# Kernel optimization log

Measured on AMD Instinct MI355X. Metric: run time of the kernel, lower is better.

The kernel has to match this reference:

```python
import jax, jax.numpy as jnp
import numpy as np

T, B, I, H, LBL = 200, 1024, 128, 128, 4


def setup_inputs() -> dict:
    key = jax.random.key(0)
    ks = jax.random.split(key, 14)
    si = 1.0 / np.sqrt(I)
    sh = 1.0 / np.sqrt(H)
    inputs = jax.random.normal(ks[0], (T, B, I), jnp.float32)
    lengths = jnp.maximum(jax.random.randint(ks[1], (B,), 1, T + 1), LBL).astype(jnp.int32)
    return {
        "inputs": inputs,
        "lengths": lengths,
        "Wih_g": jax.random.normal(ks[2], (3 * H, I), jnp.float32) * si,
        "Whh_g": jax.random.normal(ks[3], (3 * H, H), jnp.float32) * sh,
        "bih_g": jax.random.normal(ks[4], (3 * H,), jnp.float32) * sh,
        "bhh_g": jax.random.normal(ks[5], (3 * H,), jnp.float32) * sh,
        "Wih_l": jax.random.normal(ks[6], (3 * H, I), jnp.float32) * si,
        "Whh_l": jax.random.normal(ks[7], (3 * H, H), jnp.float32) * sh,
        "bih_l": jax.random.normal(ks[8], (3 * H,), jnp.float32) * sh,
        "bhh_l": jax.random.normal(ks[9], (3 * H,), jnp.float32) * sh,
        "A1": jax.random.normal(ks[10], (H, H), jnp.float32) * sh,
        "A2": jax.random.normal(ks[11], (H, H), jnp.float32) * sh,
        "v1": jax.random.normal(ks[12], (1, H), jnp.float32) * sh,
        "label_len": LBL,
    }


def gru(x, Wih, Whh, bih, bhh):
    # x: [T, B, I] time-major. PyTorch GRU cell semantics.
    Bq, Hq = x.shape[1], Whh.shape[1]
    gi_all = jnp.einsum('tbi,gi->tbg', x, Wih) + bih  # precompute input projections [T,B,3H]
    def step(h, gi):
        gh = h @ Whh.T + bhh
        ir, iz, inn = jnp.split(gi, 3, axis=-1)
        hr, hz, hn = jnp.split(gh, 3, axis=-1)
        r = jax.nn.sigmoid(ir + hr)
        z = jax.nn.sigmoid(iz + hz)
        n = jnp.tanh(inn + r * hn)
        h = (1.0 - z) * n + z * h
        return h, h
    h0 = jnp.zeros((Bq, Hq), x.dtype)
    _, hs = jax.lax.scan(step, h0, gi_all)
    return hs  # [T, B, H]


def reference(inputs, lengths, Wih_g, Whh_g, bih_g, bhh_g,
              Wih_l, Whh_l, bih_l, bhh_l, A1, A2, v1, label_len):
    h_g = gru(inputs, Wih_g, Whh_g, bih_g, bhh_g)  # [T,B,H]
    h_l = gru(inputs, Wih_l, Whh_l, bih_l, bhh_l)  # [T,B,H]
    # attention score per step s: v1(sigmoid(A1 h_l + A2 h_g)), query-independent
    pre = jax.nn.sigmoid(jnp.einsum('tbh,gh->tbg', h_l, A1) +
                         jnp.einsum('tbh,gh->tbg', h_g, A2))
    scores = jnp.einsum('tbg,og->tbo', pre, v1)  # [T,B,1]
    # per-t output = cumsum_{s<=t}(score*h_l) + h_g[t]
    out = jnp.cumsum(scores * h_l, axis=0) + h_g  # [T,B,H]
    out_b = jnp.transpose(out, (1, 0, 2))  # [B,T,H]
    # gather last label_len timesteps of each sequence: h[b,k] = out[L_b-label_len+k, b]
    idx = lengths[:, None].astype(jnp.int32) - label_len + jnp.arange(label_len, dtype=jnp.int32)[None, :]
    idx = jnp.clip(idx, 0, out_b.shape[1] - 1)  # [B, label_len]
    h = jnp.take_along_axis(out_b, idx[:, :, None], axis=1)  # [B, label_len, H]
    return h
```

## Files before the change

### kernel.cpp

```cpp
#include <hip/hip_runtime.h>
#include <stdint.h>


typedef __attribute__((ext_vector_type(8))) short short8;
typedef __attribute__((ext_vector_type(4))) float float4v;

#define LDS_BARRIER() asm volatile("s_waitcnt lgkmcnt(0)\n\ts_barrier" ::: "memory")

__device__ inline float bf2f(unsigned short u){
  union { unsigned int i; float f; } v; v.i = ((unsigned int)u) << 16; return v.f;
}
__device__ inline unsigned short f2bf(float f){
  union { float f; unsigned int i; } v; v.f = f;
  unsigned int x = v.i;
  return (unsigned short)((x + 0x7fffu + ((x >> 16) & 1u)) >> 16);
}
__device__ inline unsigned int cvt_pk_bf16(float a, float b){
  unsigned int r;
  asm("v_cvt_pk_bf16_f32 %0, %1, %2" : "=v"(r) : "v"(a), "v"(b));
  return r;
}
__device__ inline float sigm(float x){ return __builtin_amdgcn_rcpf(1.0f + __expf(-x)); }

__global__ void k_prep(unsigned short* zs, float* cum,
                       const float* A1, const float* A2, unsigned short* a12)
{
  int i = blockIdx.x * blockDim.x + threadIdx.x;
  zs[i] = 0;
  cum[i] = 0.0f;
  if (i < 32768) {
    a12[i] = f2bf((i < 16384) ? A1[i] : A2[i - 16384]);
  }
}

union __align__(16) LdsU {
  struct { unsigned short hbuf[2][16][136]; unsigned short xbuf[2][16][136]; } scan;
  struct { unsigned short M1[128][136]; unsigned short M2[128][136]; } sc;
  struct { unsigned short hlL[50 * 512]; float scL[4][50]; } cm;
};

__global__ __launch_bounds__(512, 2) void k_fat(
    const float* __restrict__ x,
    const float* __restrict__ Wih_g, const float* __restrict__ Whh_g,
    const float* __restrict__ bih_g, const float* __restrict__ bhh_g,
    const float* __restrict__ Wih_l, const float* __restrict__ Whh_l,
    const float* __restrict__ bih_l, const float* __restrict__ bhh_l,
    const unsigned short* __restrict__ a12, const float* __restrict__ v1,
    const int* __restrict__ lengths,
    unsigned short* __restrict__ hl, unsigned short* __restrict__ hg,
    const unsigned short* __restrict__ zs,
    float* __restrict__ score, float* __restrict__ cum, float* __restrict__ out,
    int scan_t0, int score_t0, int cum_t0)
{
  __shared__ LdsU lds;
  int tid = threadIdx.x;
  int bid = blockIdx.x;

  if (bid < 128) {
    if (scan_t0 < 0) return;
    const int tc = 50;
    int t0 = scan_t0;
    auto& hbuf = lds.scan.hbuf;
    auto& xbuf = lds.scan.xbuf;

    int w = tid >> 6, L = tid & 63, l15 = L & 15, q = L >> 4;
    int gru = bid & 1;
    int b0 = (bid >> 1) * 16;
    const float* Wih = gru ? Wih_l : Wih_g;
    const float* Whh = gru ? Whh_l : Whh_g;
    const float* bih = gru ? bih_l : bih_g;
    const float* bhh = gru ? bhh_l : bhh_g;
    unsigned short* myseq = gru ? hl : hg;

    int col = w * 16 + l15;

    short8 Wi[3][4], Wh[3][4];
    #pragma unroll
    for (int G = 0; G < 3; G++) {
      int row = G * 128 + col;
      #pragma unroll
      for (int kf = 0; kf < 4; kf++) {
        const float4* p0 = (const float4*)(Wih + (size_t)row * 128 + kf * 32 + q * 8);
        const float4* p1 = (const float4*)(Whh + (size_t)row * 128 + kf * 32 + q * 8);
        float4 a0 = p0[0], a1 = p0[1], b0f = p1[0], b1f = p1[1];
        short8 si, sh;
        si[0]=(short)f2bf(a0.x); si[1]=(short)f2bf(a0.y); si[2]=(short)f2bf(a0.z); si[3]=(short)f2bf(a0.w);
        si[4]=(short)f2bf(a1.x); si[5]=(short)f2bf(a1.y); si[6]=(short)f2bf(a1.z); si[7]=(short)f2bf(a1.w);
        sh[0]=(short)f2bf(b0f.x); sh[1]=(short)f2bf(b0f.y); sh[2]=(short)f2bf(b0f.z); sh[3]=(short)f2bf(b0f.w);
        sh[4]=(short)f2bf(b1f.x); sh[5]=(short)f2bf(b1f.y); sh[6]=(short)f2bf(b1f.z); sh[7]=(short)f2bf(b1f.w);
        Wi[G][kf] = si; Wh[G][kf] = sh;
      }
    }
    float br  = bih[col]       + bhh[col];
    float bz  = bih[128 + col] + bhh[128 + col];
    float bin = bih[256 + col];
    float bnh = bhh[256 + col];

    const unsigned short* carry = (t0 == 0) ? zs : (myseq + (size_t)(t0 - 1) * 131072);
    float hold[4];
    #pragma unroll
    for (int r = 0; r < 4; r++) {
      int m = q * 4 + r;
      unsigned short u = carry[(size_t)(b0 + m) * 128 + col];
      hold[r] = bf2f(u);
      hbuf[0][m][col] = u;
    }
    int xrow = tid >> 5, xc4 = (tid & 31) * 4;
    size_t hoff = (size_t)b0 * 128 + xrow * 128 + xc4;
    {
      float4 x0 = ((const float4*)(x + ((size_t)t0 * 1024 + b0) * 128))[tid];
      *(uint2*)&xbuf[0][xrow][xc4] = make_uint2(cvt_pk_bf16(x0.x, x0.y), cvt_pk_bf16(x0.z, x0.w));
    }
    float4 xr = ((const float4*)(x + ((size_t)(t0 + 1) * 1024 + b0) * 128))[tid];
    __syncthreads();

    float4v cx0 = (float4v){0.f,0.f,0.f,0.f}, cx1 = cx0, cx2 = cx0;
    {
      short8 Ax[4];
      #pragma unroll
      for (int kf = 0; kf < 4; kf++) Ax[kf] = *(const short8*)&xbuf[0][l15][kf * 32 + q * 8];
      #pragma unroll
      for (int kf = 0; kf < 4; kf++) cx0 = __builtin_amdgcn_mfma_f32_16x16x32_bf16(Ax[kf], Wi[0][kf], cx0, 0,0,0);
      #pragma unroll
      for (int kf = 0; kf < 4; kf++) cx1 = __builtin_amdgcn_mfma_f32_16x16x32_bf16(Ax[kf], Wi[1][kf], cx1, 0,0,0);
      #pragma unroll
      for (int kf = 0; kf < 4; kf++) cx2 = __builtin_amdgcn_mfma_f32_16x16x32_bf16(Ax[kf], Wi[2][kf], cx2, 0,0,0);
    }
    *(uint2*)&xbuf[1][xrow][xc4] = make_uint2(cvt_pk_bf16(xr.x, xr.y), cvt_pk_bf16(xr.z, xr.w));
    xr = ((const float4*)(x + ((size_t)(t0 + 2) * 1024 + b0) * 128))[tid];
    LDS_BARRIER();

    auto step = [&](int s, int pin, int pout) {
      short8 Ah[4], Axn[4];
      #pragma unroll
      for (int kf = 0; kf < 4; kf++) Ah[kf]  = *(const short8*)&hbuf[pin][l15][kf * 32 + q * 8];
      #pragma unroll
      for (int kf = 0; kf < 4; kf++) Axn[kf] = *(const short8*)&xbuf[pout][l15][kf * 32 + q * 8];

      if (s > 0) {
        uint2 hv = *(const uint2*)&hbuf[pin][xrow][xc4];
        *(uint2*)(myseq + (size_t)(t0 + s - 1) * 131072 + hoff) = hv;
      }

      float4v rh = (float4v){0.f,0.f,0.f,0.f}, zh = rh, nh = rh;
      #pragma unroll
      for (int kf = 0; kf < 4; kf++) rh = __builtin_amdgcn_mfma_f32_16x16x32_bf16(Ah[kf], Wh[0][kf], rh, 0,0,0);
      #pragma unroll
      for (int kf = 0; kf < 4; kf++) zh = __builtin_amdgcn_mfma_f32_16x16x32_bf16(Ah[kf], Wh[1][kf], zh, 0,0,0);
      #pragma unroll
      for (int kf = 0; kf < 4; kf++) nh = __builtin_amdgcn_mfma_f32_16x16x32_bf16(Ah[kf], Wh[2][kf], nh, 0,0,0);

      float4v nx0 = (float4v){0.f,0.f,0.f,0.f}, nx1 = nx0, nx2 = nx0;
      #pragma unroll
      for (int kf = 0; kf < 4; kf++) nx0 = __builtin_amdgcn_mfma_f32_16x16x32_bf16(Axn[kf], Wi[0][kf], nx0, 0,0,0);
      #pragma unroll
      for (int kf = 0; kf < 4; kf++) nx1 = __builtin_amdgcn_mfma_f32_16x16x32_bf16(Axn[kf], Wi[1][kf], nx1, 0,0,0);
      #pragma unroll
      for (int kf = 0; kf < 4; kf++) nx2 = __builtin_amdgcn_mfma_f32_16x16x32_bf16(Axn[kf], Wi[2][kf], nx2, 0,0,0);

      *(uint2*)&xbuf[pin][xrow][xc4] = make_uint2(cvt_pk_bf16(xr.x, xr.y), cvt_pk_bf16(xr.z, xr.w));
      {
        int t3 = t0 + (s + 3 < tc ? s + 3 : tc - 1);
        xr = ((const float4*)(x + ((size_t)t3 * 1024 + b0) * 128))[tid];
      }

      float cr[4], cz[4], cn[4];
      #pragma unroll
      for (int r = 0; r < 4; r++) { cr[r] = cx0[r] + br; cz[r] = cx1[r] + bz; cn[r] = cx2[r] + bin; }

      float hnv[4];
      #pragma unroll
      for (int r = 0; r < 4; r++) {
        float er = __expf(-(rh[r] + cr[r]));
        float ez = __expf(-(zh[r] + cz[r]));
        float pr = 1.0f + er, pz = 1.0f + ez;
        float inv = __builtin_amdgcn_rcpf(pr * pz);
        float rr = pz * inv;
        float zz = pr * inv;
        float y  = cn[r] + rr * (nh[r] + bnh);
        float em = __expf(-2.0f * y);
        float nn = 2.0f * __builtin_amdgcn_rcpf(1.0f + em) - 1.0f;
        hnv[r] = nn + zz * (hold[r] - nn);
        hold[r] = hnv[r];
      }
      unsigned int p01 = cvt_pk_bf16(hnv[0], hnv[1]);
      unsigned int p23 = cvt_pk_bf16(hnv[2], hnv[3]);
      hbuf[pout][q * 4 + 0][col] = (unsigned short)p01;
      hbuf[pout][q * 4 + 1][col] = (unsigned short)(p01 >> 16);
      hbuf[pout][q * 4 + 2][col] = (unsigned short)p23;
      hbuf[pout][q * 4 + 3][col] = (unsigned short)(p23 >> 16);

      cx0 = nx0; cx1 = nx1; cx2 = nx2;
      LDS_BARRIER();
    };

    for (int s = 0; s + 1 < tc; s += 2) { step(s, 0, 1); step(s + 1, 1, 0); }
    {
      uint2 hv = *(const uint2*)&hbuf[tc & 1][xrow][xc4];
      *(uint2*)(myseq + (size_t)(t0 + tc - 1) * 131072 + hoff) = hv;
    }
    return;
  }

  if (bid < 228) {
    if (score_t0 < 0) return;
    int rb = bid - 128;
    int w = tid >> 6, L = tid & 63;
    int l15 = L & 15, q = L >> 4;
    int s = score_t0 + (rb >> 1);
    int bhalf = (rb & 1) * 512;
    auto& M1 = lds.sc.M1;
    auto& M2 = lds.sc.M2;

    #pragma unroll
    for (int it = 0; it < 4; it++) {
      int f8 = it * 512 + tid;
      *(short8*)&M1[f8 >> 4][(f8 & 15) * 8] = *(const short8*)(a12 + (size_t)f8 * 8);
      *(short8*)&M2[f8 >> 4][(f8 & 15) * 8] = *(const short8*)(a12 + 16384 + (size_t)f8 * 8);
    }
    __syncthreads();

    float v1v[8];
    #pragma unroll
    for (int nt = 0; nt < 8; nt++) v1v[nt] = v1[nt * 16 + l15];

    short8 Fl[4], Fg[4], Pl[4], Pg[4];
    {
      size_t base = ((size_t)s * 1024 + bhalf + (size_t)w * 16 + l15) * 128;
      #pragma unroll
      for (int kf = 0; kf < 4; kf++) {
        Fl[kf] = *(const short8*)(hl + base + kf * 32 + q * 8);
        Fg[kf] = *(const short8*)(hg + base + kf * 32 + q * 8);
      }
    }
    #pragma unroll
    for (int it = 0; it < 4; it++) {
      int b0s = bhalf + (it * 8 + w) * 16;
      if (it + 1 < 4) {
        size_t base = ((size_t)s * 1024 + bhalf + (size_t)((it + 1) * 8 + w) * 16 + l15) * 128;
        #pragma unroll
        for (int kf = 0; kf < 4; kf++) {
          Pl[kf] = *(const short8*)(hl + base + kf * 32 + q * 8);
          Pg[kf] = *(const short8*)(hg + base + kf * 32 + q * 8);
        }
      }
      float4v acc[8];
      #pragma unroll
      for (int nt = 0; nt < 8; nt++) {
        float4v a = (float4v){0.f, 0.f, 0.f, 0.f};
        #pragma unroll
        for (int kf = 0; kf < 4; kf++)
          a = __builtin_amdgcn_mfma_f32_16x16x32_bf16(
              Fl[kf], *(const short8*)&M1[nt * 16 + l15][kf * 32 + q * 8], a, 0, 0, 0);
        #pragma unroll
        for (int kf = 0; kf < 4; kf++)
          a = __builtin_amdgcn_mfma_f32_16x16x32_bf16(
              Fg[kf], *(const short8*)&M2[nt * 16 + l15][kf * 32 + q * 8], a, 0, 0, 0);
        acc[nt] = a;
      }
      float p4[4];
      #pragma unroll
      for (int r = 0; r < 4; r++) {
        float sum = 0.f;
        #pragma unroll
        for (int nt = 0; nt < 8; nt++) sum += v1v[nt] * sigm(acc[nt][r]);
        sum += __shfl_xor(sum, 1, 16);
        sum += __shfl_xor(sum, 2, 16);
        sum += __shfl_xor(sum, 4, 16);
        sum += __shfl_xor(sum, 8, 16);
        p4[r] = sum;
      }
      if (l15 == 0) {
        #pragma unroll
        for (int r = 0; r < 4; r++)
          score[(size_t)(b0s + q * 4 + r) * 200 + s] = p4[r];
      }
      #pragma unroll
      for (int kf = 0; kf < 4; kf++) { Fl[kf] = Pl[kf]; Fg[kf] = Pg[kf]; }
    }
    return;
  }

  if (cum_t0 < 0) return;
  {
    int rb = bid - 228;
    int b4 = tid >> 7, j = tid & 127;
    int b0c = rb * 4;
    int b = b0c + b4;
    int t0c = cum_t0;

    float c = cum[(size_t)b * 128 + j];
    int cap0 = lengths[b] - 4;

    float hgv[4];
    #pragma unroll
    for (int d = 0; d < 4; d++) {
      int sl = cap0 + d - t0c;
      hgv[d] = (sl >= 0 && sl < 50) ? bf2f(hg[((size_t)(cap0 + d) * 1024 + b) * 128 + j]) : 0.f;
    }

    for (int f8 = tid; f8 < 50 * 64; f8 += 512) {
      int sl = f8 >> 6, r8 = f8 & 63;
      *(short8*)&lds.cm.hlL[(size_t)f8 * 8] =
          *(const short8*)(hl + ((size_t)(t0c + sl) * 1024 + b0c) * 128 + r8 * 8);
    }
    for (int i = tid; i < 4 * 50; i += 512) {
      int bb = i / 50, sl = i - bb * 50;
      lds.cm.scL[bb][sl] = score[(size_t)(b0c + bb) * 200 + t0c + sl];
    }
    __syncthreads();

    int base = b4 * 128 + j;
    for (int sl = 0; sl < 50; sl += 5) {
      float h[5], scv[5];
      #pragma unroll
      for (int k = 0; k < 5; k++) {
        h[k] = bf2f(lds.cm.hlL[(size_t)(sl + k) * 512 + base]);
        scv[k] = lds.cm.scL[b4][sl + k];
      }
      #pragma unroll
      for (int k = 0; k < 5; k++) {
        c += scv[k] * h[k];
        int d = (t0c + sl + k) - cap0;
        if ((unsigned)d < 4u)
          out[((size_t)b * 4 + d) * 128 + j] = c + hgv[d];
      }
    }
    cum[(size_t)b * 128 + j] = c;
  }
}

extern "C" void kernel_launch(void* const* d_in, const int* in_sizes, int n_in,
                              void* d_out, int out_size, void* d_ws, size_t ws_size,
                              hipStream_t stream)
{
  const float* x     = (const float*)d_in[0];
  const int* lengths = (const int*)d_in[1];
  const float* Wih_g = (const float*)d_in[2];
  const float* Whh_g = (const float*)d_in[3];
  const float* bih_g = (const float*)d_in[4];
  const float* bhh_g = (const float*)d_in[5];
  const float* Wih_l = (const float*)d_in[6];
  const float* Whh_l = (const float*)d_in[7];
  const float* bih_l = (const float*)d_in[8];
  const float* bhh_l = (const float*)d_in[9];
  const float* A1    = (const float*)d_in[10];
  const float* A2    = (const float*)d_in[11];
  const float* v1    = (const float*)d_in[12];
  float* out = (float*)d_out;

  const int TC = 50;
  char* wsb = (char*)d_ws;
  size_t o = 0;
  unsigned short* a12 = (unsigned short*)(wsb + o); o += 65536;
  float* cum          = (float*)(wsb + o);          o += 524288;
  unsigned short* zs  = (unsigned short*)(wsb + o); o += 262144;
  unsigned short* hl  = (unsigned short*)(wsb + o); o += (size_t)200 * 1024 * 128 * 2;
  unsigned short* hg  = (unsigned short*)(wsb + o); o += (size_t)200 * 1024 * 128 * 2;
  float* score        = (float*)(wsb + o);          o += (size_t)1024 * 200 * 4;
  if (o > ws_size) return;

  k_prep<<<512, 256, 0, stream>>>(zs, cum, A1, A2, a12);

  for (int Lh = 0; Lh < 6; Lh++) {
    int st0 = (Lh < 4) ? Lh * TC : -1;
    int sc0 = (Lh >= 1 && Lh <= 4) ? (Lh - 1) * TC : -1;
    int cu0 = (Lh >= 2) ? (Lh - 2) * TC : -1;
    k_fat<<<484, 512, 0, stream>>>(x, Wih_g, Whh_g, bih_g, bhh_g,
                                   Wih_l, Whh_l, bih_l, bhh_l,
                                   a12, v1, lengths, hl, hg, zs,
                                   score, cum, out, st0, sc0, cu0);
  }
}
```

Measured before the change: 421.2 us.

## Repipeline GRU scan into 100-step chunks with pre-swizzled bf16 weights

Changes the software pipeline from six launches of 50-step chunks to four launches of 100-step chunks. Score blocks now cover 100 timesteps and cumsum blocks loop over two 50-step segments. GRU weights are converted to bf16 once in the prep kernel, in the MFMA fragment layout, so each scan block does a plain vector load. The zero-state buffer is replaced by direct zero initialisation. This cuts per-launch overhead and redundant weight conversion, but the scan phases now overlap less with score and cumsum work and the pipeline fill and drain get longer.

```diff
diff --git a/kernel.cpp b/kernel.cpp
--- a/kernel.cpp
+++ b/kernel.cpp
@@ -22,14 +22,25 @@
 }
 __device__ inline float sigm(float x){ return __builtin_amdgcn_rcpf(1.0f + __expf(-x)); }
 
-__global__ void k_prep(unsigned short* zs, float* cum,
-                       const float* A1, const float* A2, unsigned short* a12)
+__global__ void k_prep(float* cum, const float* A1, const float* A2, unsigned short* a12,
+                       const float* Wih_g, const float* Whh_g,
+                       const float* Wih_l, const float* Whh_l, unsigned short* wst)
 {
   int i = blockIdx.x * blockDim.x + threadIdx.x;
-  zs[i] = 0;
-  cum[i] = 0.0f;
-  if (i < 32768) {
-    a12[i] = f2bf((i < 16384) ? A1[i] : A2[i - 16384]);
+  if (i < 131072) cum[i] = 0.0f;
+  if (i < 32768) a12[i] = f2bf((i < 16384) ? A1[i] : A2[i - 16384]);
+  {
+    int f = i >> 12;
+    int r = i & 4095;
+    int t = r >> 3, e = r & 7;
+    int l15 = t & 15, q = (t >> 4) & 3, wv = t >> 6;
+    int col = wv * 16 + l15;
+    int kf = f & 3, g3 = f >> 2;
+    int G = g3 % 3, gm = g3 / 3;
+    const float* src = (gm == 0) ? Wih_g : (gm == 1) ? Whh_g : (gm == 2) ? Wih_l : Whh_l;
+    int row = G * 128 + col;
+    int k = kf * 32 + q * 8 + e;
+    wst[i] = f2bf(src[(size_t)row * 128 + k]);
   }
 }
 
@@ -41,14 +52,12 @@
 
 __global__ __launch_bounds__(512, 2) void k_fat(
     const float* __restrict__ x,
-    const float* __restrict__ Wih_g, const float* __restrict__ Whh_g,
     const float* __restrict__ bih_g, const float* __restrict__ bhh_g,
-    const float* __restrict__ Wih_l, const float* __restrict__ Whh_l,
     const float* __restrict__ bih_l, const float* __restrict__ bhh_l,
+    const unsigned short* __restrict__ wst,
     const unsigned short* __restrict__ a12, const float* __restrict__ v1,
     const int* __restrict__ lengths,
     unsigned short* __restrict__ hl, unsigned short* __restrict__ hg,
-    const unsigned short* __restrict__ zs,
     float* __restrict__ score, float* __restrict__ cum, float* __restrict__ out,
     int scan_t0, int score_t0, int cum_t0)
 {
@@ -58,7 +67,7 @@
 
   if (bid < 128) {
     if (scan_t0 < 0) return;
-    const int tc = 50;
+    const int tc = 100;
     int t0 = scan_t0;
     auto& hbuf = lds.scan.hbuf;
     auto& xbuf = lds.scan.xbuf;
@@ -66,8 +75,6 @@
     int w = tid >> 6, L = tid & 63, l15 = L & 15, q = L >> 4;
     int gru = bid & 1;
     int b0 = (bid >> 1) * 16;
-    const float* Wih = gru ? Wih_l : Wih_g;
-    const float* Whh = gru ? Whh_l : Whh_g;
     const float* bih = gru ? bih_l : bih_g;
     const float* bhh = gru ? bhh_l : bhh_g;
     unsigned short* myseq = gru ? hl : hg;
@@ -75,20 +82,16 @@
     int col = w * 16 + l15;
 
     short8 Wi[3][4], Wh[3][4];
-    #pragma unroll
-    for (int G = 0; G < 3; G++) {
-      int row = G * 128 + col;
-      #pragma unroll
-      for (int kf = 0; kf < 4; kf++) {
-        const float4* p0 = (const float4*)(Wih + (size_t)row * 128 + kf * 32 + q * 8);
-        const float4* p1 = (const float4*)(Whh + (size_t)row * 128 + kf * 32 + q * 8);
-        float4 a0 = p0[0], a1 = p0[1], b0f = p1[0], b1f = p1[1];
-        short8 si, sh;
-        si[0]=(short)f2bf(a0.x); si[1]=(short)f2bf(a0.y); si[2]=(short)f2bf(a0.z); si[3]=(short)f2bf(a0.w);
-        si[4]=(short)f2bf(a1.x); si[5]=(short)f2bf(a1.y); si[6]=(short)f2bf(a1.z); si[7]=(short)f2bf(a1.w);
-        sh[0]=(short)f2bf(b0f.x); sh[1]=(short)f2bf(b0f.y); sh[2]=(short)f2bf(b0f.z); sh[3]=(short)f2bf(b0f.w);
-        sh[4]=(short)f2bf(b1f.x); sh[5]=(short)f2bf(b1f.y); sh[6]=(short)f2bf(b1f.z); sh[7]=(short)f2bf(b1f.w);
-        Wi[G][kf] = si; Wh[G][kf] = sh;
+    {
+      int gmi = gru * 2;
+      int gmh = gru * 2 + 1;
+      #pragma unroll
+      for (int G = 0; G < 3; G++) {
+        #pragma unroll
+        for (int kf = 0; kf < 4; kf++) {
+          Wi[G][kf] = *(const short8*)(wst + (((size_t)((gmi * 3 + G) * 4 + kf)) << 12) + tid * 8);
+          Wh[G][kf] = *(const short8*)(wst + (((size_t)((gmh * 3 + G) * 4 + kf)) << 12) + tid * 8);
+        }
       }
     }
     float br  = bih[col]       + bhh[col];
@@ -96,14 +99,19 @@
     float bin = bih[256 + col];
     float bnh = bhh[256 + col];
 
-    const unsigned short* carry = (t0 == 0) ? zs : (myseq + (size_t)(t0 - 1) * 131072);
     float hold[4];
-    #pragma unroll
-    for (int r = 0; r < 4; r++) {
-      int m = q * 4 + r;
-      unsigned short u = carry[(size_t)(b0 + m) * 128 + col];
-      hold[r] = bf2f(u);
-      hbuf[0][m][col] = u;
+    if (t0 == 0) {
+      #pragma unroll
+      for (int r = 0; r < 4; r++) { hold[r] = 0.0f; hbuf[0][q * 4 + r][col] = 0; }
+    } else {
+      const unsigned short* carry = myseq + (size_t)(t0 - 1) * 131072;
+      #pragma unroll
+      for (int r = 0; r < 4; r++) {
+        int m = q * 4 + r;
+        unsigned short u = carry[(size_t)(b0 + m) * 128 + col];
+        hold[r] = bf2f(u);
+        hbuf[0][m][col] = u;
+      }
     }
     int xrow = tid >> 5, xc4 = (tid & 31) * 4;
     size_t hoff = (size_t)b0 * 128 + xrow * 128 + xc4;
@@ -202,7 +210,7 @@
     return;
   }
 
-  if (bid < 228) {
+  if (bid < 328) {
     if (score_t0 < 0) return;
     int rb = bid - 128;
     int w = tid >> 6, L = tid & 63;
@@ -283,47 +291,51 @@
 
   if (cum_t0 < 0) return;
   {
-    int rb = bid - 228;
+    int rb = bid - 328;
     int b4 = tid >> 7, j = tid & 127;
     int b0c = rb * 4;
     int b = b0c + b4;
-    int t0c = cum_t0;
+    int base = b4 * 128 + j;
 
     float c = cum[(size_t)b * 128 + j];
     int cap0 = lengths[b] - 4;
 
-    float hgv[4];
-    #pragma unroll
-    for (int d = 0; d < 4; d++) {
-      int sl = cap0 + d - t0c;
-      hgv[d] = (sl >= 0 && sl < 50) ? bf2f(hg[((size_t)(cap0 + d) * 1024 + b) * 128 + j]) : 0.f;
-    }
-
-    for (int f8 = tid; f8 < 50 * 64; f8 += 512) {
-      int sl = f8 >> 6, r8 = f8 & 63;
-      *(short8*)&lds.cm.hlL[(size_t)f8 * 8] =
-          *(const short8*)(hl + ((size_t)(t0c + sl) * 1024 + b0c) * 128 + r8 * 8);
-    }
-    for (int i = tid; i < 4 * 50; i += 512) {
-      int bb = i / 50, sl = i - bb * 50;
-      lds.cm.scL[bb][sl] = score[(size_t)(b0c + bb) * 200 + t0c + sl];
-    }
-    __syncthreads();
-
-    int base = b4 * 128 + j;
-    for (int sl = 0; sl < 50; sl += 5) {
-      float h[5], scv[5];
-      #pragma unroll
-      for (int k = 0; k < 5; k++) {
-        h[k] = bf2f(lds.cm.hlL[(size_t)(sl + k) * 512 + base]);
-        scv[k] = lds.cm.scL[b4][sl + k];
-      }
-      #pragma unroll
-      for (int k = 0; k < 5; k++) {
-        c += scv[k] * h[k];
-        int d = (t0c + sl + k) - cap0;
-        if ((unsigned)d < 4u)
-          out[((size_t)b * 4 + d) * 128 + j] = c + hgv[d];
+    for (int seg = 0; seg < 2; seg++) {
+      int t0s = cum_t0 + seg * 50;
+      __syncthreads();
+
+      float hgv[4];
+      #pragma unroll
+      for (int d = 0; d < 4; d++) {
+        int sl = cap0 + d - t0s;
+        hgv[d] = (sl >= 0 && sl < 50) ? bf2f(hg[((size_t)(cap0 + d) * 1024 + b) * 128 + j]) : 0.f;
+      }
+
+      for (int f8 = tid; f8 < 50 * 64; f8 += 512) {
+        int sl = f8 >> 6, r8 = f8 & 63;
+        *(short8*)&lds.cm.hlL[(size_t)f8 * 8] =
+            *(const short8*)(hl + ((size_t)(t0s + sl) * 1024 + b0c) * 128 + r8 * 8);
+      }
+      for (int i = tid; i < 4 * 50; i += 512) {
+        int bb = i / 50, sl = i - bb * 50;
+        lds.cm.scL[bb][sl] = score[(size_t)(b0c + bb) * 200 + t0s + sl];
+      }
+      __syncthreads();
+
+      for (int sl = 0; sl < 50; sl += 5) {
+        float h[5], scv[5];
+        #pragma unroll
+        for (int k = 0; k < 5; k++) {
+          h[k] = bf2f(lds.cm.hlL[(size_t)(sl + k) * 512 + base]);
+          scv[k] = lds.cm.scL[b4][sl + k];
+        }
+        #pragma unroll
+        for (int k = 0; k < 5; k++) {
+          c += scv[k] * h[k];
+          int d = (t0s + sl + k) - cap0;
+          if ((unsigned)d < 4u)
+            out[((size_t)b * 4 + d) * 128 + j] = c + hgv[d];
+        }
       }
     }
     cum[(size_t)b * 128 + j] = c;
@@ -349,26 +361,24 @@
   const float* v1    = (const float*)d_in[12];
   float* out = (float*)d_out;
 
-  const int TC = 50;
   char* wsb = (char*)d_ws;
   size_t o = 0;
   unsigned short* a12 = (unsigned short*)(wsb + o); o += 65536;
   float* cum          = (float*)(wsb + o);          o += 524288;
-  unsigned short* zs  = (unsigned short*)(wsb + o); o += 262144;
+  unsigned short* wst = (unsigned short*)(wsb + o); o += 393216;
   unsigned short* hl  = (unsigned short*)(wsb + o); o += (size_t)200 * 1024 * 128 * 2;
   unsigned short* hg  = (unsigned short*)(wsb + o); o += (size_t)200 * 1024 * 128 * 2;
   float* score        = (float*)(wsb + o);          o += (size_t)1024 * 200 * 4;
   if (o > ws_size) return;
 
-  k_prep<<<512, 256, 0, stream>>>(zs, cum, A1, A2, a12);
-
-  for (int Lh = 0; Lh < 6; Lh++) {
-    int st0 = (Lh < 4) ? Lh * TC : -1;
-    int sc0 = (Lh >= 1 && Lh <= 4) ? (Lh - 1) * TC : -1;
-    int cu0 = (Lh >= 2) ? (Lh - 2) * TC : -1;
-    k_fat<<<484, 512, 0, stream>>>(x, Wih_g, Whh_g, bih_g, bhh_g,
-                                   Wih_l, Whh_l, bih_l, bhh_l,
-                                   a12, v1, lengths, hl, hg, zs,
-                                   score, cum, out, st0, sc0, cu0);
-  }
-}
+  k_prep<<<768, 256, 0, stream>>>(cum, A1, A2, a12, Wih_g, Whh_g, Wih_l, Whh_l, wst);
+
+  k_fat<<<128, 512, 0, stream>>>(x, bih_g, bhh_g, bih_l, bhh_l, wst, a12, v1, lengths,
+                                 hl, hg, score, cum, out, 0, -1, -1);
+  k_fat<<<328, 512, 0, stream>>>(x, bih_g, bhh_g, bih_l, bhh_l, wst, a12, v1, lengths,
+                                 hl, hg, score, cum, out, 100, 0, -1);
+  k_fat<<<584, 512, 0, stream>>>(x, bih_g, bhh_g, bih_l, bhh_l, wst, a12, v1, lengths,
+                                 hl, hg, score, cum, out, -1, 100, 0);
+  k_fat<<<584, 512, 0, stream>>>(x, bih_g, bhh_g, bih_l, bhh_l, wst, a12, v1, lengths,
+                                 hl, hg, score, cum, out, -1, -1, 100);
+}
```

New measurement: 398.8 us. -5.3%, faster.
